# Optimization experiments

Measured on AMD Instinct MI355X. Metric: run time of the kernel, lower is better.

Reference implementation:

```python
import jax, jax.numpy as jnp
import numpy as np
import math

B, L, D, H, DK, DFF = 4, 1024, 1024, 16, 64, 4096
NUM_BUCKETS, MAX_DIST = 32, 128


def _relative_position_bucket(rel):
    # bidirectional T5 bucketing; rel = memory_pos - context_pos
    nb = NUM_BUCKETS // 2
    n = -rel
    ret = (n < 0).astype(jnp.int32) * nb
    n = jnp.abs(n)
    max_exact = nb // 2
    is_small = n < max_exact
    val_if_large = max_exact + (
        jnp.log(jnp.maximum(n, 1).astype(jnp.float32) / max_exact)
        / math.log(MAX_DIST / max_exact)
        * (nb - max_exact)
    ).astype(jnp.int32)
    val_if_large = jnp.minimum(val_if_large, nb - 1)
    return ret + jnp.where(is_small, n.astype(jnp.int32), val_if_large)


def t5_layernorm(x, w, eps):
    # no mean subtraction, no bias (T5 style)
    var = jnp.mean(jnp.square(x.astype(jnp.float32)), axis=-1, keepdims=True)
    return w * (x / jnp.sqrt(var + eps))


def setup_inputs() -> dict:
    key = jax.random.key(0)
    ks = jax.random.split(key, 12)
    inp = {
        "src": jax.random.normal(ks[0], (B, L, D), dtype=jnp.float32),
        "enc_position": jnp.broadcast_to(jnp.arange(L, dtype=jnp.int32), (B, L)),
        "ln1_w": jnp.ones((D,), jnp.float32),
        "wq": jax.random.normal(ks[1], (H * DK, D), jnp.float32) * (D * DK) ** -0.5,
        "bq": jnp.zeros((H * DK,), jnp.float32),
        "wk": jax.random.normal(ks[2], (H * DK, D), jnp.float32) * D ** -0.5,
        "bk": jnp.zeros((H * DK,), jnp.float32),
        "wv": jax.random.normal(ks[3], (H * DK, D), jnp.float32) * D ** -0.5,
        "bv": jnp.zeros((H * DK,), jnp.float32),
        "fc_w": jax.random.normal(ks[4], (D, H * DK), jnp.float32) * (H * DK) ** -0.5,
        "fc_b": jnp.zeros((D,), jnp.float32),
        "rel_bias": jax.random.normal(ks[5], (NUM_BUCKETS, H), jnp.float32) * 0.02,
        "ln2_w": jnp.ones((D,), jnp.float32),
        "wi": jax.random.normal(ks[6], (DFF, D), jnp.float32) * D ** -0.5,
        "wo": jax.random.normal(ks[7], (D, DFF), jnp.float32) * DFF ** -0.5,
    }
    return inp


def reference(src, enc_position, ln1_w, wq, bq, wk, bk, wv, bv, fc_w, fc_b,
              rel_bias, ln2_w, wi, wo):
    b, l, d = src.shape
    temp = DK ** 0.5

    # --- Multi-head self attention (pre-LN, T5 relative bias) ---
    proj = t5_layernorm(src, ln1_w, 1e-12)
    q = (proj @ wq.T + bq).reshape(b, l, H, DK).transpose(0, 2, 1, 3)  # [b,h,l,dk]
    k = (proj @ wk.T + bk).reshape(b, l, H, DK).transpose(0, 2, 1, 3)
    v = (proj @ wv.T + bv).reshape(b, l, H, DK).transpose(0, 2, 1, 3)

    # relative position bias: [b, h, l_q, l_k]
    rel = enc_position[:, None, :] - enc_position[:, :, None]  # mem - ctx
    bucket = _relative_position_bucket(rel)                    # [b, l, l]
    position_bias = rel_bias[bucket].transpose(0, 3, 1, 2)     # [b, h, l, l]

    scores = jnp.einsum("bhqd,bhkd->bhqk", q / temp, k) + position_bias
    attn = jax.nn.softmax(scores, axis=-1)                     # dropout = eval no-op
    ctx = jnp.einsum("bhqk,bhkd->bhqd", attn, v)
    ctx = ctx.transpose(0, 2, 1, 3).reshape(b, l, H * DK)
    attn_out = ctx @ fc_w.T + fc_b + src                       # residual
    attn_sum = jnp.sum(attn, axis=1)                           # [b, l, l]

    # --- Position-wise FFN (pre-LN, gelu, no biases) ---
    nx = t5_layernorm(attn_out, ln2_w, 1e-6)
    h = jax.nn.gelu(nx @ wi.T, approximate=False)
    out = attn_out + h @ wo.T
    return out, attn_sum, position_bias
```

## Files before the change

### kernel.cpp

```cpp
#include <hip/hip_runtime.h>
#include <hip/hip_bf16.h>
#include <math.h>

typedef __attribute__((ext_vector_type(8))) short short8;
typedef __attribute__((ext_vector_type(4))) float f32x4;
typedef unsigned short u16;

#define L2E 1.44269504088896340736f

__device__ __forceinline__ u16 f2bf(float f) {
  union { float f; unsigned u; } x; x.f = f;
  unsigned r = x.u + 0x7fffu + ((x.u >> 16) & 1u);
  return (u16)(r >> 16);
}

__device__ __forceinline__ void gload16(const void* g, void* l) {
  auto gp = reinterpret_cast<const __attribute__((address_space(1))) void*>(
      reinterpret_cast<uintptr_t>(g));
  auto lp = reinterpret_cast<__attribute__((address_space(3))) void*>(
      reinterpret_cast<uintptr_t>(l));
  __builtin_amdgcn_global_load_lds(gp, lp, 16, 0, 0);
}

__device__ __forceinline__ int xcd_swz(int flat, int nwg) {
  return (flat & 7) * (nwg >> 3) + (flat >> 3);
}

__device__ __forceinline__ int bucket_fn(int rel) {
  int n = -rel;
  int ret = 0;
  if (n < 0) { ret = 16; n = -n; }
  if (n < 8) return ret + n;
  int e = 31 - __clz(n);
  unsigned nn = (unsigned)n * (unsigned)n;
  int f = 2 * e + ((nn >= (1u << (2 * e + 1))) ? 1 : 0) - 6;
  int val = 8 + f;
  if (val > 15) val = 15;
  return ret + val;
}

__global__ __launch_bounds__(256) void prep(
    const float* __restrict__ wq, const float* __restrict__ wk,
    const float* __restrict__ wv, const float* __restrict__ fcw,
    const float* __restrict__ wi, const float* __restrict__ wo,
    const float* __restrict__ bq, const float* __restrict__ bk,
    const float* __restrict__ bv, const float* __restrict__ rel_bias,
    u16* __restrict__ wqb, u16* __restrict__ wkb, u16* __restrict__ wvb,
    u16* __restrict__ fcwb, u16* __restrict__ wib, u16* __restrict__ wob,
    float* __restrict__ fb, float* __restrict__ tab) {
  const int blk = blockIdx.x, t = threadIdx.x;
  if (blk < 12288) {
    const float* s; u16* d; int rel;
    if (blk < 1024)      { s = wq;  d = wqb;  rel = blk; }
    else if (blk < 2048) { s = wk;  d = wkb;  rel = blk - 1024; }
    else if (blk < 3072) { s = wv;  d = wvb;  rel = blk - 2048; }
    else if (blk < 4096) { s = fcw; d = fcwb; rel = blk - 3072; }
    else if (blk < 8192) { s = wi;  d = wib;  rel = blk - 4096; }
    else                 { s = wo;  d = wob;  rel = blk - 8192; }
    const int i = (rel * 256 + t) * 4;
    float4 v = *(const float4*)&s[i];
    d[i + 0] = f2bf(v.x); d[i + 1] = f2bf(v.y);
    d[i + 2] = f2bf(v.z); d[i + 3] = f2bf(v.w);
  } else if (blk < 12300) {
    const int i = (blk - 12288) * 256 + t;
    fb[i] = i < 1024 ? bq[i] : (i < 2048 ? bk[i - 1024] : bv[i - 2048]);
  } else {
    const int idx = (blk - 12300) * 256 + t;
    const int h = idx >> 11;
    const int rel = (idx & 2047) - 1024;
    tab[idx] = rel_bias[bucket_fn(rel) * 16 + h];
  }
}

__global__ __launch_bounds__(256) void t5_ln(const float* __restrict__ x,
                                             const float* __restrict__ wgt,
                                             float eps, u16* __restrict__ out) {
  const int row = blockIdx.x, t = threadIdx.x;
  const float4 v = ((const float4*)(x + (size_t)row * 1024))[t];
  float ss = v.x * v.x + v.y * v.y + v.z * v.z + v.w * v.w;
#pragma unroll
  for (int off = 1; off < 64; off <<= 1) ss += __shfl_xor(ss, off, 64);
  __shared__ float red[4];
  if ((t & 63) == 0) red[t >> 6] = ss;
  __syncthreads();
  float tot = red[0] + red[1] + red[2] + red[3];
  float inv = 1.0f / sqrtf(tot * (1.0f / 1024.0f) + eps);
  const float4 wv = ((const float4*)wgt)[t];
  u16* o = out + (size_t)row * 1024 + t * 4;
  o[0] = f2bf(v.x * inv * wv.x);
  o[1] = f2bf(v.y * inv * wv.y);
  o[2] = f2bf(v.z * inv * wv.z);
  o[3] = f2bf(v.w * inv * wv.w);
}

__global__ __launch_bounds__(256) void transpose_v(const u16* __restrict__ v,
                                                   u16* __restrict__ vt) {
  __shared__ u16 T[64][72];
  const int bh = blockIdx.y;
  const int l0 = blockIdx.x * 64;
  const int t = threadIdx.x;
  const int sr = t >> 3, sc = (t & 7) * 8;
  const u16* vb = v + (size_t)bh * 65536;
  *(short8*)&T[sr][sc]      = *(const short8*)&vb[(size_t)(l0 + sr) * 64 + sc];
  *(short8*)&T[sr + 32][sc] = *(const short8*)&vb[(size_t)(l0 + sr + 32) * 64 + sc];
  __syncthreads();
  u16* vtb = vt + (size_t)bh * 65536;
  short8 o0, o1;
#pragma unroll
  for (int u = 0; u < 8; u++) {
    ((u16*)&o0)[u] = T[sc + u][sr];
    ((u16*)&o1)[u] = T[sc + u][sr + 32];
  }
  *(short8*)&vtb[(size_t)sr * 1024 + l0 + sc]        = o0;
  *(short8*)&vtb[(size_t)(sr + 32) * 1024 + l0 + sc] = o1;
}

template<int MODE>
__global__ __launch_bounds__(256, 3) void gemm_nt(
    const u16* __restrict__ A, const u16* __restrict__ Bw,
    int M, int N, int K,
    const float* __restrict__ bias, const float* __restrict__ res,
    float scale, float* __restrict__ outF, u16* __restrict__ outB) {
  __shared__ u16 As[3][4096];
  __shared__ u16 Bs[3][4096];
  const int t = threadIdx.x;
  const int w = t >> 6, lane = t & 63;
  const int wr = w >> 1, wc = w & 1;
  const int g = lane >> 4, lc = lane & 15;

  const int nwg = gridDim.x * gridDim.y;
  const int flat = xcd_swz(blockIdx.y * gridDim.x + blockIdx.x, nwg);
  const int bx = flat % gridDim.x, by = flat / gridDim.x;
  const int m0 = by * 128, n0 = bx * 128;

  const int srow = w * 16 + (lane >> 2);
  const int sc8  = (lane & 3) ^ ((srow >> 1) & 3);
  const u16* Ag = &A[(size_t)(m0 + srow) * K + sc8 * 8];
  const u16* Bg = &Bw[(size_t)(n0 + srow) * K + sc8 * 8];
  const size_t row64 = (size_t)64 * K;
  const int swz = (lc >> 1) & 3;

  const int NT = K >> 5;
  f32x4 acc[4][4] = {};

  auto stage = [&](int buf, int tt) {
    const int k0 = tt << 5;
    u16* lA = &As[buf][w * 512];
    u16* lB = &Bs[buf][w * 512];
    gload16(Ag + k0, lA);
    gload16(Ag + row64 + k0, lA + 2048);
    gload16(Bg + k0, lB);
    gload16(Bg + row64 + k0, lB + 2048);
  };

  stage(0, 0);
  stage(1, 1);

  for (int tt = 0; tt < NT; tt++) {
    const int cur = tt % 3;
    if (tt < NT - 1) {
      asm volatile("s_waitcnt vmcnt(4)" ::: "memory");
    } else {
      asm volatile("s_waitcnt vmcnt(0)" ::: "memory");
    }
    __builtin_amdgcn_s_barrier();
    if (tt + 2 < NT) stage((tt + 2) % 3, tt + 2);
    short8 af[4], bf[4];
#pragma unroll
    for (int mi = 0; mi < 4; mi++)
      af[mi] = *(short8*)&As[cur][(wr * 64 + mi * 16 + lc) * 32 + (g ^ swz) * 8];
#pragma unroll
    for (int ni = 0; ni < 4; ni++)
      bf[ni] = *(short8*)&Bs[cur][(wc * 64 + ni * 16 + lc) * 32 + (g ^ swz) * 8];
#pragma unroll
    for (int mi = 0; mi < 4; mi++)
#pragma unroll
      for (int ni = 0; ni < 4; ni++)
        acc[mi][ni] = __builtin_amdgcn_mfma_f32_16x16x32_bf16(af[mi], bf[ni], acc[mi][ni], 0, 0, 0);
  }

  u16* Es = &As[0][0];
  __syncthreads();
#pragma unroll
  for (int mi = 0; mi < 4; mi++) {
#pragma unroll
    for (int ni = 0; ni < 4; ni++) {
#pragma unroll
      for (int r = 0; r < 4; r++) {
        const int col = n0 + wc * 64 + ni * 16 + lc;
        float v = acc[mi][ni][r];
        if (MODE == 0) {
          v = (v + bias[col]) * ((col >> 10) == 0 ? scale : 1.0f);
        } else {
          v = 0.5f * v * (1.0f + erff(v * 0.70710678118654752440f));
        }
        Es[wr * 2048 + (g * 4 + r) * 128 + wc * 64 + ni * 16 + lc] = f2bf(v);
      }
    }
    __syncthreads();
    {
      const int rr = t >> 3;
      const int wr2 = rr >> 4, r16 = rr & 15;
      const int cc = (t & 7) * 16;
      short8 o0 = *(short8*)&Es[wr2 * 2048 + r16 * 128 + cc];
      short8 o1 = *(short8*)&Es[wr2 * 2048 + r16 * 128 + cc + 8];
      const int row = m0 + wr2 * 64 + mi * 16 + r16;
      if (MODE == 0) {
        const int col0 = n0 + cc;
        const int which = col0 >> 10, c = col0 & 1023;
        const int hh = c >> 6, dk = c & 63;
        const int b = row >> 10, pos = row & 1023;
        u16* dst = outB + (size_t)which * 4194304 +
                   (((size_t)(b * 16 + hh)) * 1024 + pos) * 64 + dk;
        *(short8*)dst = o0;
        *(short8*)(dst + 8) = o1;
      } else {
        u16* dst = outB + (size_t)row * (size_t)N + n0 + cc;
        *(short8*)dst = o0;
        *(short8*)(dst + 8) = o1;
      }
    }
    __syncthreads();
  }
}

template<int MODE>
__global__ __launch_bounds__(256, 4) void gemm_nt64(
    const u16* __restrict__ A, const u16* __restrict__ Bw,
    int M, int N, int K,
    const float* __restrict__ bias, const float* __restrict__ res,
    float* __restrict__ outF) {
  __shared__ u16 As[3][2048];
  __shared__ u16 Bs[3][4096];
  const int t = threadIdx.x;
  const int w = t >> 6, lane = t & 63;
  const int wr = w >> 1, wc = w & 1;
  const int g = lane >> 4, lc = lane & 15;

  const int nwg = gridDim.x * gridDim.y;
  const int flat = xcd_swz(blockIdx.y * gridDim.x + blockIdx.x, nwg);
  const int bx = flat % gridDim.x, by = flat / gridDim.x;
  const int m0 = by * 64, n0 = bx * 128;

  const int srow = w * 16 + (lane >> 2);
  const int sc8  = (lane & 3) ^ ((srow >> 1) & 3);
  const u16* Ag = &A[(size_t)(m0 + srow) * K + sc8 * 8];
  const u16* Bg = &Bw[(size_t)(n0 + srow) * K + sc8 * 8];
  const size_t row64 = (size_t)64 * K;
  const int swz = (lc >> 1) & 3;

  const int NT = K >> 5;
  f32x4 acc[2][4] = {};

  auto stage = [&](int buf, int tt) {
    const int k0 = tt << 5;
    gload16(Ag + k0, &As[buf][w * 512]);
    gload16(Bg + k0, &Bs[buf][w * 512]);
    gload16(Bg + row64 + k0, &Bs[buf][w * 512 + 2048]);
  };

  stage(0, 0);
  stage(1, 1);

  for (int tt = 0; tt < NT; tt++) {
    const int cur = tt % 3;
    if (tt < NT - 1) {
      asm volatile("s_waitcnt vmcnt(3)" ::: "memory");
    } else {
      asm volatile("s_waitcnt vmcnt(0)" ::: "memory");
    }
    __builtin_amdgcn_s_barrier();
    if (tt + 2 < NT) stage((tt + 2) % 3, tt + 2);
    short8 af[2], bf[4];
#pragma unroll
    for (int mi = 0; mi < 2; mi++)
      af[mi] = *(short8*)&As[cur][(wr * 32 + mi * 16 + lc) * 32 + (g ^ swz) * 8];
#pragma unroll
    for (int ni = 0; ni < 4; ni++)
      bf[ni] = *(short8*)&Bs[cur][(wc * 64 + ni * 16 + lc) * 32 + (g ^ swz) * 8];
#pragma unroll
    for (int mi = 0; mi < 2; mi++)
#pragma unroll
      for (int ni = 0; ni < 4; ni++)
        acc[mi][ni] = __builtin_amdgcn_mfma_f32_16x16x32_bf16(af[mi], bf[ni], acc[mi][ni], 0, 0, 0);
  }

#pragma unroll
  for (int mi = 0; mi < 2; mi++) {
#pragma unroll
    for (int ni = 0; ni < 4; ni++) {
#pragma unroll
      for (int r = 0; r < 4; r++) {
        const int row = m0 + wr * 32 + mi * 16 + g * 4 + r;
        const int col = n0 + wc * 64 + ni * 16 + lc;
        float v = acc[mi][ni][r];
        if (MODE == 1) {
          v += bias[col] + res[(size_t)row * 1024 + col];
        } else {
          v += res[(size_t)row * 1024 + col];
        }
        outF[(size_t)row * 1024 + col] = v;
      }
    }
  }
}

__global__ __launch_bounds__(256) void attn_kernel(
    const u16* __restrict__ q, const u16* __restrict__ k,
    const u16* __restrict__ vt, const float* __restrict__ tab,
    u16* __restrict__ ctx, float* __restrict__ ml, float* __restrict__ pb) {
  const int flat = xcd_swz(blockIdx.y * 16 + blockIdx.x, 1024);
  const int bh = flat / 16;
  const int i0 = (flat % 16) * 64;
  const int h = bh & 15, b = bh >> 4;
  const int t = threadIdx.x, w = t >> 6, lane = t & 63;
  const int g = lane >> 4, lc = lane & 15;
  const int sr = t >> 3;
  const int swc = ((t & 7) ^ (sr & 7)) * 8;
  const int sc = (t & 7) * 8;

  __shared__ u16 Ks[2][64][64];
  __shared__ u16 Vts[2][64][64];
  __shared__ u16 P[4][16][64];
  __shared__ float tabs[2048];

  const u16* qb  = q + (size_t)bh * 65536;
  const u16* kb  = k + (size_t)bh * 65536;
  const u16* vtb = vt + (size_t)bh * 65536;

  ((float4*)tabs)[t]       = ((const float4*)(tab + h * 2048))[t];
  ((float4*)tabs)[t + 256] = ((const float4*)(tab + h * 2048))[t + 256];

  const short8 aq0 = *(const short8*)&qb[(size_t)(i0 + w * 16 + lc) * 64 + g * 8];
  const short8 aq1 = *(const short8*)&qb[(size_t)(i0 + w * 16 + lc) * 64 + 32 + g * 8];

  {
    short8 ka = *(const short8*)&kb[(size_t)sr * 64 + sc];
    short8 kc = *(const short8*)&kb[(size_t)(sr + 32) * 64 + sc];
    short8 va = *(const short8*)&vtb[(size_t)sr * 1024 + sc];
    short8 vc = *(const short8*)&vtb[(size_t)(sr + 32) * 1024 + sc];
    *(short8*)&Ks[0][sr][swc]       = ka;
    *(short8*)&Ks[0][sr + 32][swc]  = kc;
    *(short8*)&Vts[0][sr][swc]      = va;
    *(short8*)&Vts[0][sr + 32][swc] = vc;
  }
  __syncthreads();

  const int rx = lc & 7;
  const int ibase = 1024 - i0 - (w * 16 + g * 4) + lc;
  float* pbrow = pb + (size_t)bh * 1048576 + (size_t)i0 * 1024 + t * 4;

  float m_r[4] = {-INFINITY, -INFINITY, -INFINITY, -INFINITY};
  float l_r[4] = {0.f, 0.f, 0.f, 0.f};
  f32x4 cacc[4] = {};

  for (int tt = 0; tt < 16; tt++) {
    const int buf = tt & 1;
    const int j0 = tt * 64;

    short8 nka, nkc, nva, nvc;
    if (tt < 15) {
      const int jn = j0 + 64;
      nka = *(const short8*)&kb[(size_t)(jn + sr) * 64 + sc];
      nkc = *(const short8*)&kb[(size_t)(jn + sr + 32) * 64 + sc];
      nva = *(const short8*)&vtb[(size_t)sr * 1024 + jn + sc];
      nvc = *(const short8*)&vtb[(size_t)(sr + 32) * 1024 + jn + sc];
    }

    f32x4 s[4] = {};
#pragma unroll
    for (int ni = 0; ni < 4; ni++) {
      short8 b0 = *(short8*)&Ks[buf][ni * 16 + lc][(g ^ rx) * 8];
      short8 b1 = *(short8*)&Ks[buf][ni * 16 + lc][((4 + g) ^ rx) * 8];
      s[ni] = __builtin_amdgcn_mfma_f32_16x16x32_bf16(aq0, b0, s[ni], 0, 0, 0);
      s[ni] = __builtin_amdgcn_mfma_f32_16x16x32_bf16(aq1, b1, s[ni], 0, 0, 0);
    }
#pragma unroll
    for (int ni = 0; ni < 4; ni++)
#pragma unroll
      for (int r = 0; r < 4; r++)
        s[ni][r] = fmaf(tabs[ibase + j0 + ni * 16 - r], L2E, s[ni][r]);

#pragma unroll
    for (int r = 0; r < 4; r++) {
      float tm = fmaxf(fmaxf(s[0][r], s[1][r]), fmaxf(s[2][r], s[3][r]));
#pragma unroll
      for (int off = 1; off < 16; off <<= 1) tm = fmaxf(tm, __shfl_xor(tm, off, 64));
      const float mn = fmaxf(m_r[r], tm);
      const float scl = __builtin_amdgcn_exp2f(m_r[r] - mn);
      float rs = 0.f;
#pragma unroll
      for (int ni = 0; ni < 4; ni++) {
        float p = __builtin_amdgcn_exp2f(s[ni][r] - mn);
        s[ni][r] = p;
        rs += p;
      }
#pragma unroll
      for (int off = 1; off < 16; off <<= 1) rs += __shfl_xor(rs, off, 64);
      l_r[r] = l_r[r] * scl + rs;
      m_r[r] = mn;
#pragma unroll
      for (int d = 0; d < 4; d++) cacc[d][r] *= scl;
    }

#pragma unroll
    for (int ni = 0; ni < 4; ni++)
#pragma unroll
      for (int r = 0; r < 4; r++) {
        const int prow = g * 4 + r;
        P[w][prow][(((ni * 2 + (lc >> 3)) ^ (prow & 7)) << 3) | (lc & 7)] = f2bf(s[ni][r]);
      }

    short8 ap0 = *(short8*)&P[w][lc][(g ^ rx) * 8];
    short8 ap1 = *(short8*)&P[w][lc][((4 + g) ^ rx) * 8];
#pragma unroll
    for (int d = 0; d < 4; d++) {
      short8 bv0 = *(short8*)&Vts[buf][d * 16 + lc][(g ^ rx) * 8];
      short8 bv1 = *(short8*)&Vts[buf][d * 16 + lc][((4 + g) ^ rx) * 8];
      cacc[d] = __builtin_amdgcn_mfma_f32_16x16x32_bf16(ap0, bv0, cacc[d], 0, 0, 0);
      cacc[d] = __builtin_amdgcn_mfma_f32_16x16x32_bf16(ap1, bv1, cacc[d], 0, 0, 0);
    }

    {
#pragma unroll
      for (int r4 = 0; r4 < 4; r4++) {
        const int il = tt * 4 + r4;
        const int base = t * 4 - (i0 + il) + 1024;
        float4 o;
        o.x = tabs[base + 0];
        o.y = tabs[base + 1];
        o.z = tabs[base + 2];
        o.w = tabs[base + 3];
        *(float4*)&pbrow[(size_t)il * 1024] = o;
      }
    }

    if (tt < 15) {
      *(short8*)&Ks[buf ^ 1][sr][swc]       = nka;
      *(short8*)&Ks[buf ^ 1][sr + 32][swc]  = nkc;
      *(short8*)&Vts[buf ^ 1][sr][swc]      = nva;
      *(short8*)&Vts[buf ^ 1][sr + 32][swc] = nvc;
    }
    __syncthreads();
  }

  float inv[4];
#pragma unroll
  for (int r = 0; r < 4; r++) inv[r] = 1.0f / l_r[r];
#pragma unroll
  for (int d = 0; d < 4; d++)
#pragma unroll
    for (int r = 0; r < 4; r++) {
      const int pos = i0 + w * 16 + g * 4 + r;
      ctx[((size_t)b * 1024 + pos) * 1024 + h * 64 + d * 16 + lc] = f2bf(cacc[d][r] * inv[r]);
    }
  if (lc == 0) {
#pragma unroll
    for (int r = 0; r < 4; r++) {
      const int i = i0 + w * 16 + g * 4 + r;
      ml[(size_t)bh * 1024 + i] = m_r[r];
      ml[65536 + (size_t)bh * 1024 + i] = l_r[r];
    }
  }
}

__global__ __launch_bounds__(256) void attn_sum_kernel(
    const u16* __restrict__ q, const u16* __restrict__ k,
    const float* __restrict__ tab, const float* __restrict__ ml,
    float* __restrict__ asum) {
  const int flat = xcd_swz(((blockIdx.z * 16 + blockIdx.y) * 16) + blockIdx.x, 1024);
  const int j0 = (flat % 16) * 64;
  const int i0 = ((flat / 16) % 16) * 64;
  const int b = flat / 256;
  const int t = threadIdx.x, w = t >> 6, lane = t & 63;
  const int g = lane >> 4, lc = lane & 15;
  const int sr = t >> 3;
  const int swc = ((t & 7) ^ (sr & 7)) * 8;
  const int sc = (t & 7) * 8;
  const int rx = lc & 7;
  __shared__ u16 Ks[64][64];
  __shared__ float tabs[128];

  f32x4 acc[4] = {};

  for (int h = 0; h < 16; h++) {
    const int bh = b * 16 + h;
    __syncthreads();
    const u16* kb = k + (size_t)bh * 65536;
    *(short8*)&Ks[sr][swc]      = *(const short8*)&kb[(size_t)(j0 + sr) * 64 + sc];
    *(short8*)&Ks[sr + 32][swc] = *(const short8*)&kb[(size_t)(j0 + sr + 32) * 64 + sc];
    if (t < 127) tabs[t] = tab[h * 2048 + (j0 - i0 - 63 + t) + 1024] * L2E;
    __syncthreads();
    const u16* qb = q + (size_t)bh * 65536;
    short8 aq0 = *(const short8*)&qb[(size_t)(i0 + w * 16 + lc) * 64 + g * 8];
    short8 aq1 = *(const short8*)&qb[(size_t)(i0 + w * 16 + lc) * 64 + 32 + g * 8];
    f32x4 s[4] = {};
#pragma unroll
    for (int ni = 0; ni < 4; ni++) {
      short8 b0 = *(short8*)&Ks[ni * 16 + lc][(g ^ rx) * 8];
      short8 b1 = *(short8*)&Ks[ni * 16 + lc][((4 + g) ^ rx) * 8];
      s[ni] = __builtin_amdgcn_mfma_f32_16x16x32_bf16(aq0, b0, s[ni], 0, 0, 0);
      s[ni] = __builtin_amdgcn_mfma_f32_16x16x32_bf16(aq1, b1, s[ni], 0, 0, 0);
    }
    float mm[4], li[4];
#pragma unroll
    for (int r = 0; r < 4; r++) {
      const int i = i0 + w * 16 + g * 4 + r;
      mm[r] = ml[(size_t)bh * 1024 + i];
      li[r] = 1.0f / ml[65536 + (size_t)bh * 1024 + i];
    }
#pragma unroll
    for (int ni = 0; ni < 4; ni++)
#pragma unroll
      for (int r = 0; r < 4; r++) {
        float sv = s[ni][r] + tabs[ni * 16 + lc - w * 16 - g * 4 - r + 63];
        acc[ni][r] += __builtin_amdgcn_exp2f(sv - mm[r]) * li[r];
      }
  }
#pragma unroll
  for (int ni = 0; ni < 4; ni++)
#pragma unroll
    for (int r = 0; r < 4; r++) {
      const int i = i0 + w * 16 + g * 4 + r;
      asum[((size_t)b * 1024 + i) * 1024 + j0 + ni * 16 + lc] = acc[ni][r];
    }
}

extern "C" void kernel_launch(void* const* d_in, const int* in_sizes, int n_in,
                              void* d_out, int out_size, void* d_ws, size_t ws_size,
                              hipStream_t stream) {
  const float* src      = (const float*)d_in[0];
  const float* ln1_w    = (const float*)d_in[2];
  const float* wq       = (const float*)d_in[3];
  const float* bq       = (const float*)d_in[4];
  const float* wk       = (const float*)d_in[5];
  const float* bk       = (const float*)d_in[6];
  const float* wv       = (const float*)d_in[7];
  const float* bv       = (const float*)d_in[8];
  const float* fc_w     = (const float*)d_in[9];
  const float* fc_b     = (const float*)d_in[10];
  const float* rel_bias = (const float*)d_in[11];
  const float* ln2_w    = (const float*)d_in[12];
  const float* wi       = (const float*)d_in[13];
  const float* wo       = (const float*)d_in[14];

  const size_t MB = 1u << 20;
  char* ws = (char*)d_ws;
  u16* wq_b   = (u16*)(ws + 0 * MB);
  u16* wk_b   = (u16*)(ws + 2 * MB);
  u16* wv_b   = (u16*)(ws + 4 * MB);
  u16* fcw_b  = (u16*)(ws + 6 * MB);
  u16* wi_b   = (u16*)(ws + 8 * MB);
  u16* wo_b   = (u16*)(ws + 16 * MB);
  u16* proj_b = (u16*)(ws + 24 * MB);
  u16* q_b    = (u16*)(ws + 32 * MB);
  u16* k_b    = (u16*)(ws + 40 * MB);
  u16* v_b    = (u16*)(ws + 48 * MB);
  u16* vt_b   = (u16*)(ws + 56 * MB);
  u16* h_b    = (u16*)(ws + 32 * MB);
  u16* ctx_b  = (u16*)(ws + 64 * MB);
  float* attn_out = (float*)(ws + 72 * MB);
  float* ml   = (float*)(ws + 88 * MB);
  float* tab  = (float*)(ws + 88 * MB + 512 * 1024);
  float* fb   = (float*)(ws + 90 * MB);

  float* outF = (float*)d_out;
  float* asum = outF + 4194304;
  float* pb   = outF + 8388608;

  prep<<<12428, 256, 0, stream>>>(wq, wk, wv, fc_w, wi, wo, bq, bk, bv, rel_bias,
                                  wq_b, wk_b, wv_b, fcw_b, wi_b, wo_b, fb, tab);

  t5_ln<<<4096, 256, 0, stream>>>(src, ln1_w, 1e-12f, proj_b);

  gemm_nt<0><<<dim3(24, 32), 256, 0, stream>>>(proj_b, wq_b, 4096, 3072, 1024, fb, nullptr,
                                               0.125f * L2E, nullptr, q_b);

  transpose_v<<<dim3(16, 64), 256, 0, stream>>>(v_b, vt_b);
  attn_kernel<<<dim3(16, 64), 256, 0, stream>>>(q_b, k_b, vt_b, tab, ctx_b, ml, pb);
  attn_sum_kernel<<<dim3(16, 16, 4), 256, 0, stream>>>(q_b, k_b, tab, ml, asum);

  gemm_nt64<1><<<dim3(8, 64), 256, 0, stream>>>(ctx_b, fcw_b, 4096, 1024, 1024, fc_b, src, attn_out);

  t5_ln<<<4096, 256, 0, stream>>>(attn_out, ln2_w, 1e-6f, proj_b);

  gemm_nt<2><<<dim3(32, 32), 256, 0, stream>>>(proj_b, wi_b, 4096, 4096, 1024, nullptr, nullptr,
                                               1.0f, nullptr, h_b);
  gemm_nt64<3><<<dim3(8, 64), 256, 0, stream>>>(h_b, wo_b, 4096, 1024, 4096, nullptr, attn_out, outF);
}
```

Before: 329.8 us.

## Co-schedule fc projection GEMM with attn_sum and fold LN1 into prep

Merges the first layernorm into the weight-conversion prep kernel as extra blocks, saving one launch. Also fuses the fc output projection GEMM (512 blocks) and the independent attention-sum recomputation (1024 blocks) into one launch with block-index dispatch. Both halves then run concurrently and fill the GPU better than two small serial kernels. The cost is a shared LDS pool sized for the larger half and a 3-blocks-per-SM launch bound that applies to both.

```diff
diff --git a/kernel.cpp b/kernel.cpp
--- a/kernel.cpp
+++ b/kernel.cpp
@@ -39,7 +39,7 @@
   return ret + val;
 }
 
-__global__ __launch_bounds__(256) void prep(
+__global__ __launch_bounds__(256) void prep_ln(
     const float* __restrict__ wq, const float* __restrict__ wk,
     const float* __restrict__ wv, const float* __restrict__ fcw,
     const float* __restrict__ wi, const float* __restrict__ wo,
@@ -47,7 +47,9 @@
     const float* __restrict__ bv, const float* __restrict__ rel_bias,
     u16* __restrict__ wqb, u16* __restrict__ wkb, u16* __restrict__ wvb,
     u16* __restrict__ fcwb, u16* __restrict__ wib, u16* __restrict__ wob,
-    float* __restrict__ fb, float* __restrict__ tab) {
+    float* __restrict__ fb, float* __restrict__ tab,
+    const float* __restrict__ src, const float* __restrict__ ln1_w,
+    u16* __restrict__ proj) {
   const int blk = blockIdx.x, t = threadIdx.x;
   if (blk < 12288) {
     const float* s; u16* d; int rel;
@@ -64,11 +66,28 @@
   } else if (blk < 12300) {
     const int i = (blk - 12288) * 256 + t;
     fb[i] = i < 1024 ? bq[i] : (i < 2048 ? bk[i - 1024] : bv[i - 2048]);
-  } else {
+  } else if (blk < 12428) {
     const int idx = (blk - 12300) * 256 + t;
     const int h = idx >> 11;
     const int rel = (idx & 2047) - 1024;
     tab[idx] = rel_bias[bucket_fn(rel) * 16 + h];
+  } else {
+    const int row = blk - 12428;
+    const float4 v = ((const float4*)(src + (size_t)row * 1024))[t];
+    float ss = v.x * v.x + v.y * v.y + v.z * v.z + v.w * v.w;
+#pragma unroll
+    for (int off = 1; off < 64; off <<= 1) ss += __shfl_xor(ss, off, 64);
+    __shared__ float red[4];
+    if ((t & 63) == 0) red[t >> 6] = ss;
+    __syncthreads();
+    float tot = red[0] + red[1] + red[2] + red[3];
+    float inv = 1.0f / sqrtf(tot * (1.0f / 1024.0f) + 1e-12f);
+    const float4 wv = ((const float4*)ln1_w)[t];
+    u16* o = proj + (size_t)row * 1024 + t * 4;
+    o[0] = f2bf(v.x * inv * wv.x);
+    o[1] = f2bf(v.y * inv * wv.y);
+    o[2] = f2bf(v.z * inv * wv.z);
+    o[3] = f2bf(v.w * inv * wv.w);
   }
 }
 
@@ -305,6 +324,141 @@
   }
 }
 
+__global__ __launch_bounds__(256, 3) void fc_asum(
+    const u16* __restrict__ ctx, const u16* __restrict__ fcw,
+    const float* __restrict__ fc_b, const float* __restrict__ src,
+    float* __restrict__ attn_out,
+    const u16* __restrict__ q, const u16* __restrict__ k,
+    const float* __restrict__ tab, const float* __restrict__ ml,
+    float* __restrict__ asum) {
+  __shared__ char pool[36864];
+  const int t = threadIdx.x;
+  const int w = t >> 6, lane = t & 63;
+  const int g = lane >> 4, lc = lane & 15;
+
+  if (blockIdx.x < 512) {
+    u16* As = (u16*)pool;
+    u16* Bs = (u16*)(pool + 12288);
+    const int wr = w >> 1, wc = w & 1;
+    const int flat = xcd_swz(blockIdx.x, 512);
+    const int bx = flat & 7, by = flat >> 3;
+    const int m0 = by * 64, n0 = bx * 128;
+    const int K = 1024;
+
+    const int srow = w * 16 + (lane >> 2);
+    const int sc8  = (lane & 3) ^ ((srow >> 1) & 3);
+    const u16* Ag = &ctx[(size_t)(m0 + srow) * K + sc8 * 8];
+    const u16* Bg = &fcw[(size_t)(n0 + srow) * K + sc8 * 8];
+    const size_t row64 = (size_t)64 * K;
+    const int swz = (lc >> 1) & 3;
+
+    const int NT = K >> 5;
+    f32x4 acc[2][4] = {};
+
+    auto stage = [&](int buf, int tt) {
+      const int k0 = tt << 5;
+      gload16(Ag + k0, &As[buf * 2048 + w * 512]);
+      gload16(Bg + k0, &Bs[buf * 4096 + w * 512]);
+      gload16(Bg + row64 + k0, &Bs[buf * 4096 + w * 512 + 2048]);
+    };
+
+    stage(0, 0);
+    stage(1, 1);
+
+    for (int tt = 0; tt < NT; tt++) {
+      const int cur = tt % 3;
+      if (tt < NT - 1) {
+        asm volatile("s_waitcnt vmcnt(3)" ::: "memory");
+      } else {
+        asm volatile("s_waitcnt vmcnt(0)" ::: "memory");
+      }
+      __builtin_amdgcn_s_barrier();
+      if (tt + 2 < NT) stage((tt + 2) % 3, tt + 2);
+      short8 af[2], bf[4];
+#pragma unroll
+      for (int mi = 0; mi < 2; mi++)
+        af[mi] = *(short8*)&As[cur * 2048 + (wr * 32 + mi * 16 + lc) * 32 + (g ^ swz) * 8];
+#pragma unroll
+      for (int ni = 0; ni < 4; ni++)
+        bf[ni] = *(short8*)&Bs[cur * 4096 + (wc * 64 + ni * 16 + lc) * 32 + (g ^ swz) * 8];
+#pragma unroll
+      for (int mi = 0; mi < 2; mi++)
+#pragma unroll
+        for (int ni = 0; ni < 4; ni++)
+          acc[mi][ni] = __builtin_amdgcn_mfma_f32_16x16x32_bf16(af[mi], bf[ni], acc[mi][ni], 0, 0, 0);
+    }
+
+#pragma unroll
+    for (int mi = 0; mi < 2; mi++) {
+#pragma unroll
+      for (int ni = 0; ni < 4; ni++) {
+#pragma unroll
+        for (int r = 0; r < 4; r++) {
+          const int row = m0 + wr * 32 + mi * 16 + g * 4 + r;
+          const int col = n0 + wc * 64 + ni * 16 + lc;
+          float v = acc[mi][ni][r] + fc_b[col] + src[(size_t)row * 1024 + col];
+          attn_out[(size_t)row * 1024 + col] = v;
+        }
+      }
+    }
+  } else {
+    u16* Ks = (u16*)pool;
+    float* tabs = (float*)(pool + 8192);
+    const int flat = xcd_swz(blockIdx.x - 512, 1024);
+    const int j0 = (flat % 16) * 64;
+    const int i0 = ((flat / 16) % 16) * 64;
+    const int b = flat / 256;
+    const int sr = t >> 3;
+    const int swc = ((t & 7) ^ (sr & 7)) * 8;
+    const int sc = (t & 7) * 8;
+    const int rx = lc & 7;
+
+    f32x4 acc[4] = {};
+
+    for (int h = 0; h < 16; h++) {
+      const int bh = b * 16 + h;
+      __syncthreads();
+      const u16* kb = k + (size_t)bh * 65536;
+      *(short8*)&Ks[sr * 64 + swc]        = *(const short8*)&kb[(size_t)(j0 + sr) * 64 + sc];
+      *(short8*)&Ks[(sr + 32) * 64 + swc] = *(const short8*)&kb[(size_t)(j0 + sr + 32) * 64 + sc];
+      if (t < 127) tabs[t] = tab[h * 2048 + (j0 - i0 - 63 + t) + 1024] * L2E;
+      __syncthreads();
+      const u16* qb = q + (size_t)bh * 65536;
+      short8 aq0 = *(const short8*)&qb[(size_t)(i0 + w * 16 + lc) * 64 + g * 8];
+      short8 aq1 = *(const short8*)&qb[(size_t)(i0 + w * 16 + lc) * 64 + 32 + g * 8];
+      f32x4 s[4] = {};
+#pragma unroll
+      for (int ni = 0; ni < 4; ni++) {
+        short8 b0 = *(short8*)&Ks[(ni * 16 + lc) * 64 + (g ^ rx) * 8];
+        short8 b1 = *(short8*)&Ks[(ni * 16 + lc) * 64 + ((4 + g) ^ rx) * 8];
+        s[ni] = __builtin_amdgcn_mfma_f32_16x16x32_bf16(aq0, b0, s[ni], 0, 0, 0);
+        s[ni] = __builtin_amdgcn_mfma_f32_16x16x32_bf16(aq1, b1, s[ni], 0, 0, 0);
+      }
+      float mm[4], li[4];
+#pragma unroll
+      for (int r = 0; r < 4; r++) {
+        const int i = i0 + w * 16 + g * 4 + r;
+        mm[r] = ml[(size_t)bh * 1024 + i];
+        li[r] = 1.0f / ml[65536 + (size_t)bh * 1024 + i];
+      }
+#pragma unroll
+      for (int ni = 0; ni < 4; ni++)
+#pragma unroll
+        for (int r = 0; r < 4; r++) {
+          float sv = s[ni][r] + tabs[ni * 16 + lc - w * 16 - g * 4 - r + 63];
+          acc[ni][r] += __builtin_amdgcn_exp2f(sv - mm[r]) * li[r];
+        }
+    }
+#pragma unroll
+    for (int ni = 0; ni < 4; ni++)
+#pragma unroll
+      for (int r = 0; r < 4; r++) {
+        const int i = i0 + w * 16 + g * 4 + r;
+        asum[((size_t)b * 1024 + i) * 1024 + j0 + ni * 16 + lc] = acc[ni][r];
+      }
+  }
+}
+
 __global__ __launch_bounds__(256) void attn_kernel(
     const u16* __restrict__ q, const u16* __restrict__ k,
     const u16* __restrict__ vt, const float* __restrict__ tab,
@@ -462,68 +616,6 @@
       ml[65536 + (size_t)bh * 1024 + i] = l_r[r];
     }
   }
-}
-
-__global__ __launch_bounds__(256) void attn_sum_kernel(
-    const u16* __restrict__ q, const u16* __restrict__ k,
-    const float* __restrict__ tab, const float* __restrict__ ml,
-    float* __restrict__ asum) {
-  const int flat = xcd_swz(((blockIdx.z * 16 + blockIdx.y) * 16) + blockIdx.x, 1024);
-  const int j0 = (flat % 16) * 64;
-  const int i0 = ((flat / 16) % 16) * 64;
-  const int b = flat / 256;
-  const int t = threadIdx.x, w = t >> 6, lane = t & 63;
-  const int g = lane >> 4, lc = lane & 15;
-  const int sr = t >> 3;
-  const int swc = ((t & 7) ^ (sr & 7)) * 8;
-  const int sc = (t & 7) * 8;
-  const int rx = lc & 7;
-  __shared__ u16 Ks[64][64];
-  __shared__ float tabs[128];
-
-  f32x4 acc[4] = {};
-
-  for (int h = 0; h < 16; h++) {
-    const int bh = b * 16 + h;
-    __syncthreads();
-    const u16* kb = k + (size_t)bh * 65536;
-    *(short8*)&Ks[sr][swc]      = *(const short8*)&kb[(size_t)(j0 + sr) * 64 + sc];
-    *(short8*)&Ks[sr + 32][swc] = *(const short8*)&kb[(size_t)(j0 + sr + 32) * 64 + sc];
-    if (t < 127) tabs[t] = tab[h * 2048 + (j0 - i0 - 63 + t) + 1024] * L2E;
-    __syncthreads();
-    const u16* qb = q + (size_t)bh * 65536;
-    short8 aq0 = *(const short8*)&qb[(size_t)(i0 + w * 16 + lc) * 64 + g * 8];
-    short8 aq1 = *(const short8*)&qb[(size_t)(i0 + w * 16 + lc) * 64 + 32 + g * 8];
-    f32x4 s[4] = {};
-#pragma unroll
-    for (int ni = 0; ni < 4; ni++) {
-      short8 b0 = *(short8*)&Ks[ni * 16 + lc][(g ^ rx) * 8];
-      short8 b1 = *(short8*)&Ks[ni * 16 + lc][((4 + g) ^ rx) * 8];
-      s[ni] = __builtin_amdgcn_mfma_f32_16x16x32_bf16(aq0, b0, s[ni], 0, 0, 0);
-      s[ni] = __builtin_amdgcn_mfma_f32_16x16x32_bf16(aq1, b1, s[ni], 0, 0, 0);
-    }
-    float mm[4], li[4];
-#pragma unroll
-    for (int r = 0; r < 4; r++) {
-      const int i = i0 + w * 16 + g * 4 + r;
-      mm[r] = ml[(size_t)bh * 1024 + i];
-      li[r] = 1.0f / ml[65536 + (size_t)bh * 1024 + i];
-    }
-#pragma unroll
-    for (int ni = 0; ni < 4; ni++)
-#pragma unroll
-      for (int r = 0; r < 4; r++) {
-        float sv = s[ni][r] + tabs[ni * 16 + lc - w * 16 - g * 4 - r + 63];
-        acc[ni][r] += __builtin_amdgcn_exp2f(sv - mm[r]) * li[r];
-      }
-  }
-#pragma unroll
-  for (int ni = 0; ni < 4; ni++)
-#pragma unroll
-    for (int r = 0; r < 4; r++) {
-      const int i = i0 + w * 16 + g * 4 + r;
-      asum[((size_t)b * 1024 + i) * 1024 + j0 + ni * 16 + lc] = acc[ni][r];
-    }
 }
 
 extern "C" void kernel_launch(void* const* d_in, const int* in_sizes, int n_in,
@@ -568,19 +660,18 @@
   float* asum = outF + 4194304;
   float* pb   = outF + 8388608;
 
-  prep<<<12428, 256, 0, stream>>>(wq, wk, wv, fc_w, wi, wo, bq, bk, bv, rel_bias,
-                                  wq_b, wk_b, wv_b, fcw_b, wi_b, wo_b, fb, tab);
-
-  t5_ln<<<4096, 256, 0, stream>>>(src, ln1_w, 1e-12f, proj_b);
+  prep_ln<<<16524, 256, 0, stream>>>(wq, wk, wv, fc_w, wi, wo, bq, bk, bv, rel_bias,
+                                     wq_b, wk_b, wv_b, fcw_b, wi_b, wo_b, fb, tab,
+                                     src, ln1_w, proj_b);
 
   gemm_nt<0><<<dim3(24, 32), 256, 0, stream>>>(proj_b, wq_b, 4096, 3072, 1024, fb, nullptr,
                                                0.125f * L2E, nullptr, q_b);
 
   transpose_v<<<dim3(16, 64), 256, 0, stream>>>(v_b, vt_b);
   attn_kernel<<<dim3(16, 64), 256, 0, stream>>>(q_b, k_b, vt_b, tab, ctx_b, ml, pb);
-  attn_sum_kernel<<<dim3(16, 16, 4), 256, 0, stream>>>(q_b, k_b, tab, ml, asum);
-
-  gemm_nt64<1><<<dim3(8, 64), 256, 0, stream>>>(ctx_b, fcw_b, 4096, 1024, 1024, fc_b, src, attn_out);
+
+  fc_asum<<<1536, 256, 0, stream>>>(ctx_b, fcw_b, fc_b, src, attn_out,
+                                    q_b, k_b, tab, ml, asum);
 
   t5_ln<<<4096, 256, 0, stream>>>(attn_out, ln2_w, 1e-6f, proj_b);
 
```

New measurement: 322.8 us, median of 2. 2.1% less time.
